# Optimization experiments

Measured on AMD Instinct MI355X. Metric: run time of the kernel, lower is better.

Reference implementation:

```python
import jax, jax.numpy as jnp
import numpy as np

B, T, CIN, HID, OUT, H, W = 8, 8, 128, 64, 64, 32, 32


def _conv(x, w, b):
    # x: [B, C, H, W], w: [O, C, kh, kw] -> SAME-padded conv, stride 1
    y = jax.lax.conv_general_dilated(x, w, (1, 1), "SAME",
                                     dimension_numbers=("NCHW", "OIHW", "NCHW"))
    return y + b[None, :, None, None]


def _layer_dir(xs, w_ih, w_hh, b_ih, b_hh, reverse):
    # xs: [T, B, C, H, W]; one direction of a ConvLSTM layer; returns hs [T, B, HID, H, W]
    b, hh_, ww_ = xs.shape[1], xs.shape[3], xs.shape[4]
    h0 = jnp.zeros((b, HID, hh_, ww_), xs.dtype)

    def step(carry, x):
        h, c = carry
        gates = _conv(x, w_ih, b_ih) + _conv(h, w_hh, b_hh)  # [B, 4*HID, H, W]
        i, f, g, o = jnp.split(gates, 4, axis=1)
        c = jax.nn.sigmoid(f) * c + jax.nn.sigmoid(i) * jnp.tanh(g)
        h = jax.nn.sigmoid(o) * jnp.tanh(c)
        return (h, c), h

    _, hs = jax.lax.scan(step, (h0, h0), xs, reverse=reverse)
    return hs


def _forward(features, w_ih0f, w_hh0f, b_ih0f, b_hh0f,
             w_ih0r, w_hh0r, b_ih0r, b_hh0r,
             w_ih1f, w_hh1f, b_ih1f, b_hh1f,
             w_ih1r, w_hh1r, b_ih1r, b_hh1r,
             w_out, b_out):
    xs = jnp.transpose(features, (1, 0, 2, 3, 4))  # [T, B, C, H, W]
    # layer 0, both directions (scan reverse=True aligns outputs to original time order)
    hf = _layer_dir(xs, w_ih0f, w_hh0f, b_ih0f, b_hh0f, False)
    hr = _layer_dir(xs, w_ih0r, w_hh0r, b_ih0r, b_hh0r, True)
    xs1 = jnp.concatenate([hf, hr], axis=2)  # [T, B, 2*HID, H, W] (dropout is identity at eval)
    # layer 1
    hf1 = _layer_dir(xs1, w_ih1f, w_hh1f, b_ih1f, b_hh1f, False)
    hr1 = _layer_dir(xs1, w_ih1r, w_hh1r, b_ih1r, b_hh1r, True)
    last = jnp.concatenate([hf1[-1], hr1[-1]], axis=1)  # output[:, -1] -> [B, 2*HID, H, W]
    return jax.nn.relu(_conv(last, w_out, b_out))


def setup_inputs() -> dict:
    key = jax.random.key(0)
    ks = jax.random.split(key, 24)
    G = 4 * HID
    p = lambda k, s: jax.random.normal(k, s, jnp.float32) * 0.05
    d = {"features": jax.random.normal(ks[0], (B, T, CIN, H, W), jnp.float32)}
    i = 1
    for l, cin in ((0, CIN), (1, 2 * HID)):
        for dr in ("f", "r"):
            d[f"w_ih{l}{dr}"] = p(ks[i], (G, cin, 3, 3)); i += 1
            d[f"w_hh{l}{dr}"] = p(ks[i], (G, HID, 3, 3)); i += 1
            d[f"b_ih{l}{dr}"] = p(ks[i], (G,)); i += 1
            d[f"b_hh{l}{dr}"] = p(ks[i], (G,)); i += 1
    d["w_out"] = p(ks[i], (OUT, 2 * HID, 1, 1)); i += 1
    d["b_out"] = p(ks[i], (OUT,))
    return d


def reference(features, w_ih0f, w_hh0f, b_ih0f, b_hh0f,
              w_ih0r, w_hh0r, b_ih0r, b_hh0r,
              w_ih1f, w_hh1f, b_ih1f, b_hh1f,
              w_ih1r, w_hh1r, b_ih1r, b_hh1r,
              w_out, b_out):
    return _forward(features, w_ih0f, w_hh0f, b_ih0f, b_hh0f,
                    w_ih0r, w_hh0r, b_ih0r, b_hh0r,
                    w_ih1f, w_hh1f, b_ih1f, b_hh1f,
                    w_ih1r, w_hh1r, b_ih1r, b_hh1r,
                    w_out, b_out)
```

## Files before the change

### kernel.cpp

```cpp
#include <hip/hip_runtime.h>
#include <math.h>
#include <stdint.h>


typedef __attribute__((ext_vector_type(8))) short short8;
typedef __attribute__((ext_vector_type(4))) float float4v;

namespace {
constexpr int IMG = 34 * 34 * 64;
constexpr size_t SLOTI = 16ull * IMG;
constexpr int ROWB = 34 * 128;
constexpr int PADB = 8192;
constexpr size_t GSLOT = 8ull * 256 * 1024;
constexpr int CGU32 = 73728;
}
template <int N> struct IC { static constexpr int v = N; };

__device__ __forceinline__ uint16_t bf16_rne(float x) {
  uint32_t u = __builtin_bit_cast(uint32_t, x);
  return (uint16_t)((u + 0x7FFFu + ((u >> 16) & 1u)) >> 16);
}
__device__ __forceinline__ float bf16_to_f(uint16_t h) {
  uint32_t u = ((uint32_t)h) << 16;
  return __builtin_bit_cast(float, u);
}

__device__ __forceinline__ void gl_lds16(const void* g, void* l) {
  __builtin_amdgcn_global_load_lds(
      (const __attribute__((address_space(1))) void*)g,
      (__attribute__((address_space(3))) void*)l, 16, 0, 0);
}

__global__ void pack_features(const float* __restrict__ f, uint16_t* __restrict__ out) {
  const size_t i = (size_t)blockIdx.x * 256 + threadIdx.x;
  const int blk_s = (int)(i & 7);
  size_t pp = i >> 3;
  const int px = (int)(pp % 34); pp /= 34;
  const int yy = (int)(pp % 34); pp /= 34;
  const int cg = (int)(pp & 3);
  const int bt = (int)(pp >> 2);
  const int b = bt & 7, t = bt >> 3;
  const int blk = blk_s ^ (px & 7);
  const int pl = blk >> 2, kg = blk & 3;
  short8 sv;
  if (px == 0 || px == 33 || yy == 0 || yy == 33) {
    #pragma unroll
    for (int j = 0; j < 8; ++j) sv[j] = 0;
  } else {
    const int x = px - 1, y = yy - 1;
    #pragma unroll
    for (int j = 0; j < 8; ++j) {
      const int ch = cg * 32 + kg * 8 + j;
      const float fv = f[(((size_t)b * 8 + t) * 128 + ch) * 1024 + y * 32 + x];
      const uint16_t hi = bf16_rne(fv);
      sv[j] = (short)(pl ? bf16_rne(fv - bf16_to_f(hi)) : hi);
    }
  }
  *(short8*)(out + i * 8) = sv;
}

struct WPackArgs {
  const float* wih[4]; const float* whh[4];
  const float* bih[4]; const float* bhh[4];
  uint32_t* wp; float* bp;
};
__global__ void pack_weights(WPackArgs A) {
  const int combo = blockIdx.y;
  const int idx = blockIdx.x * 256 + threadIdx.x;
  const int q = idx & 4095;
  const int rest = idx >> 12;
  const int nt = rest & 1;
  const int ct = rest >> 1;
  const int tap = ct % 9, cg = ct / 9;
  const int w2 = q & 3;
  const int b8s = (q >> 2) & 7;
  const int hcp = (q >> 5) & 15;
  const int g = (q >> 9) & 3;
  const int pl = (q >> 11) & 1;
  const int b8 = b8s ^ (hcp & 7);
  const int kg = b8 & 3;
  const int hcl = hcp * 2 + (b8 >> 2);
  const int n = g * 64 + nt * 32 + hcl;
  const float* wih = A.wih[combo];
  const float* whh = A.whh[combo];
  uint32_t out = 0;
  #pragma unroll
  for (int e = 0; e < 2; ++e) {
    const int ch = cg * 32 + kg * 8 + w2 * 2 + e;
    const float wv = (ch < 128) ? wih[((size_t)n * 128 + ch) * 9 + tap]
                                : whh[((size_t)n * 64 + (ch - 128)) * 9 + tap];
    const uint16_t hi = bf16_rne(wv);
    const uint16_t v = pl ? bf16_rne(wv - bf16_to_f(hi)) : hi;
    out |= ((uint32_t)v) << (16 * e);
  }
  A.wp[(size_t)combo * 442368 + idx] = out;
  if (idx < 256) A.bp[combo * 256 + idx] = A.bih[combo][idx] + A.bhh[combo][idx];
}

struct StepArgs {
  const uint16_t* in0; const uint16_t* in1; const uint16_t* in2;
  int nc0, nc1, nc2;
  const uint32_t* W;
  const float* bias;
  const float* gpre;
  float* cbuf;
  uint16_t* himg;
  float* hf32;
};

template <int ROWS>
__global__ __launch_bounds__(ROWS * 128, ROWS / 2) void conv_lstm_step(StepArgs A0, StepArgs A1) {
  constexpr int NW = ROWS * 2;
  constexpr int THREADS = NW * 64;
  constexpr int BANDS = 32 / ROWS;
  constexpr int LOGB = (ROWS == 4) ? 3 : 4;
  constexpr int ACH = (ROWS == 4) ? 4 : 5;
  constexpr int ASLOT = ACH * NW * 1024;
  constexpr int WCH = 16384 / (NW * 1024);
  constexpr int CNT0 = WCH;
  constexpr int CNT12 = WCH + ACH;

  extern __shared__ char smem[];
  char* Asm_ = smem;
  char* Wsm_ = smem + 2 * ASLOT;

  const StepArgs a = (blockIdx.z == 0) ? A0 : A1;
  const int bx = blockIdx.x;
  const int nt = bx & 1;
  const int band = (bx >> 1) & (BANDS - 1);
  const int b = bx >> (1 + LOGB);
  const int y0 = band * ROWS;
  const int tid = threadIdx.x;
  const int lane = tid & 63;
  const int w = tid >> 6;
  const int m15 = lane & 15;
  const int kg = lane >> 4;
  const int r = w & (ROWS - 1);
  const int hcg = (ROWS == 4) ? (w >> 2) : (w >> 1);

  int offA[2][3][2];
  #pragma unroll
  for (int xh = 0; xh < 2; ++xh)
    #pragma unroll
    for (int kx = 0; kx < 3; ++kx)
      #pragma unroll
      for (int pl = 0; pl < 2; ++pl) {
        const int px = xh * 16 + kx + m15;
        const int sw = (pl * 4 + kg) ^ (px & 7);
        offA[xh][kx][pl] = r * ROWB + px * 128 + sw * 16;
      }
  int offW[2][4];
  {
    const int hcp = hcg * 8 + (m15 >> 1);
    const int b8 = kg + 4 * (m15 & 1);
    #pragma unroll
    for (int pl = 0; pl < 2; ++pl)
      #pragma unroll
      for (int g = 0; g < 4; ++g)
        offW[pl][g] = (((pl * 4 + g) * 16 + hcp) * 8 + (b8 ^ (hcp & 7))) * 16;
  }

  const int ncg = a.nc0 + a.nc1 + a.nc2;
  auto abase = [&](int cg) -> const char* {
    const uint16_t* t;
    if (cg < a.nc0) t = a.in0 + ((size_t)b * a.nc0 + cg) * IMG;
    else if (cg < a.nc0 + a.nc1) t = a.in1 + ((size_t)b * a.nc1 + (cg - a.nc0)) * IMG;
    else t = a.in2 + ((size_t)b * a.nc2 + (cg - a.nc0 - a.nc1)) * IMG;
    return (const char*)t + (size_t)y0 * ROWB;
  };
  auto stageA = [&](int cgi, int par) {
    const char* g = abase(cgi);
    char* d = Asm_ + par * ASLOT;
    #pragma unroll
    for (int j = 0; j < ACH; ++j)
      gl_lds16(g + (size_t)(ACH * w + j) * 1024 + lane * 16, d + (ACH * w + j) * 1024);
  };
  const char* const wbeg = (const char*)a.W + (size_t)nt * 16384;
  const char* const wend = (const char*)a.W + (size_t)(ncg > 0 ? ncg : 1) * 9 * 32768;
  const char* wsrc = wbeg;
  auto stageW = [&](int slot) {
    char* d = Wsm_ + slot * 16384;
    #pragma unroll
    for (int j = 0; j < WCH; ++j)
      gl_lds16(wsrc + (size_t)(WCH * w + j) * 1024 + lane * 16, d + (WCH * w + j) * 1024);
    wsrc += 32768;
    if (wsrc >= wend) wsrc = wbeg;
  };

  float4v acc[2][4];
  #pragma unroll
  for (int xh = 0; xh < 2; ++xh)
    #pragma unroll
    for (int g = 0; g < 4; ++g) acc[xh][g] = (float4v){0.f, 0.f, 0.f, 0.f};

  if (ncg > 0) {
    stageA(0, 0);
    stageW(0);
    stageW(1);

    for (int cg = 0; cg < ncg; ++cg) {
      auto tap_body = [&](auto tapc) {
        constexpr int TAP = decltype(tapc)::v;
        constexpr int CNT = (TAP == 1 || TAP == 2) ? CNT12 : CNT0;
        constexpr int SLOT2 = (TAP + 2) % 3;
        constexpr int SLOTR = TAP % 3;
        asm volatile("s_waitcnt vmcnt(%0)\n\ts_barrier" :: "n"(CNT) : "memory");
        stageW(SLOT2);
        if (TAP == 0) {
          const int nx = (cg + 1 < ncg) ? cg + 1 : 0;
          stageA(nx, (cg + 1) & 1);
        }
        constexpr int ky = TAP / 3, kx = TAP % 3;
        const char* Ab = Asm_ + (cg & 1) * ASLOT + ky * ROWB;
        const char* Wb = Wsm_ + SLOTR * 16384;
        short8 af[2][2];
        #pragma unroll
        for (int xh = 0; xh < 2; ++xh)
          #pragma unroll
          for (int pl = 0; pl < 2; ++pl)
            af[xh][pl] = *(const short8*)(Ab + offA[xh][kx][pl]);
        short8 wfr[2][4];
        #pragma unroll
        for (int pl = 0; pl < 2; ++pl)
          #pragma unroll
          for (int g = 0; g < 4; ++g)
            wfr[pl][g] = *(const short8*)(Wb + offW[pl][g]);
        __builtin_amdgcn_s_setprio(1);
        #pragma unroll
        for (int xh = 0; xh < 2; ++xh)
          #pragma unroll
          for (int g = 0; g < 4; ++g) {
            acc[xh][g] = __builtin_amdgcn_mfma_f32_16x16x32_bf16(af[xh][0], wfr[0][g], acc[xh][g], 0, 0, 0);
            acc[xh][g] = __builtin_amdgcn_mfma_f32_16x16x32_bf16(af[xh][0], wfr[1][g], acc[xh][g], 0, 0, 0);
            acc[xh][g] = __builtin_amdgcn_mfma_f32_16x16x32_bf16(af[xh][1], wfr[0][g], acc[xh][g], 0, 0, 0);
          }
        __builtin_amdgcn_s_setprio(0);
      };
      tap_body(IC<0>{}); tap_body(IC<1>{}); tap_body(IC<2>{});
      tap_body(IC<3>{}); tap_body(IC<4>{}); tap_body(IC<5>{});
      tap_body(IC<6>{}); tap_body(IC<7>{}); tap_body(IC<8>{});
    }
    asm volatile("s_waitcnt vmcnt(0)" ::: "memory");
  }

  const int hcl = hcg * 16 + m15;
  const int hc = nt * 32 + hcl;
  const int y = y0 + r;
  float bi[4];
  #pragma unroll
  for (int g = 0; g < 4; ++g) bi[g] = a.bias[g * 64 + hc];
  float* crow = a.cbuf + ((size_t)(b * 64 + hc)) * 1024 + y * 32;
  float* hrow = a.hf32 ? a.hf32 + ((size_t)(b * 64 + hc)) * 1024 + y * 32 : nullptr;
  uint16_t* hb = a.himg ? a.himg + ((size_t)(b * 2 + nt)) * IMG : nullptr;
  const int kgb = hcl >> 3, jj = hcl & 7;
  #pragma unroll
  for (int xh = 0; xh < 2; ++xh) {
    const int x0 = xh * 16 + kg * 4;
    float4v cv = *(float4v*)(crow + x0);
    float4v pre[4];
    if (a.gpre) {
      #pragma unroll
      for (int g = 0; g < 4; ++g)
        pre[g] = *(const float4v*)(a.gpre + ((size_t)(b * 256 + g * 64 + hc)) * 1024 + y * 32 + x0);
    } else {
      #pragma unroll
      for (int g = 0; g < 4; ++g) pre[g] = (float4v){bi[g], bi[g], bi[g], bi[g]};
    }
    float4v cn, hn;
    #pragma unroll
    for (int q = 0; q < 4; ++q) {
      const float ig = 1.f / (1.f + expf(-(acc[xh][0][q] + pre[0][q])));
      const float fg = 1.f / (1.f + expf(-(acc[xh][1][q] + pre[1][q])));
      const float gg = tanhf(acc[xh][2][q] + pre[2][q]);
      const float og = 1.f / (1.f + expf(-(acc[xh][3][q] + pre[3][q])));
      const float c2 = fg * cv[q] + ig * gg;
      cn[q] = c2;
      hn[q] = og * tanhf(c2);
    }
    *(float4v*)(crow + x0) = cn;
    if (hrow) *(float4v*)(hrow + x0) = hn;
    if (hb) {
      #pragma unroll
      for (int q = 0; q < 4; ++q) {
        const int px = x0 + q + 1;
        const int sw = px & 7;
        const uint16_t hi = bf16_rne(hn[q]);
        const uint16_t lo = bf16_rne(hn[q] - bf16_to_f(hi));
        const size_t p16 = ((size_t)(y + 1) * 34 + px) * 64;
        hb[p16 + (size_t)(kgb ^ sw) * 8 + jj] = hi;
        hb[p16 + (size_t)((4 + kgb) ^ sw) * 8 + jj] = lo;
      }
    }
  }
  if (hb) {
    {
      const int rr = tid >> 7;
      const int hlf = (tid >> 6) & 1;
      const int jx = tid & 63;
      hb[((size_t)(y0 + 1 + rr) * 34 + hlf * 33) * 64 + jx] = 0;
    }
    if (band == 0) for (int i = tid; i < 2176; i += THREADS) hb[i] = 0;
    if (band == BANDS - 1) for (int i = tid; i < 2176; i += THREADS) hb[(size_t)33 * 2176 + i] = 0;
  }
}

struct PreArgs {
  const uint16_t* hf0i; const uint16_t* hr0i;
  const uint32_t* WP; const float* bp; float* gpre;
};
__global__ __launch_bounds__(512, 2) void conv_gates_pre(PreArgs P) {
  constexpr int ACH = 4, ASLOT = 32768, WCH = 2, CNT0 = 2, CNT12 = 6;
  extern __shared__ char smem[];
  char* Asm_ = smem;
  char* Wsm_ = smem + 65536;

  const int slot = blockIdx.y;
  const uint16_t* in0; const uint16_t* in1; const uint32_t* Wc; const float* bias;
  if (slot < 8) {
    in0 = P.hf0i + (size_t)(slot + 1) * SLOTI; in1 = P.hr0i + (size_t)slot * SLOTI;
    Wc = P.WP + (size_t)2 * 442368; bias = P.bp + 2 * 256;
  } else {
    in0 = P.hf0i + (size_t)8 * SLOTI; in1 = P.hr0i + (size_t)7 * SLOTI;
    Wc = P.WP + (size_t)3 * 442368; bias = P.bp + 3 * 256;
  }

  const int bx = blockIdx.x;
  const int nt = bx & 1;
  const int band = (bx >> 1) & 7;
  const int b = bx >> 4;
  const int y0 = band * 4;
  const int tid = threadIdx.x;
  const int lane = tid & 63;
  const int w = tid >> 6;
  const int m15 = lane & 15;
  const int kg = lane >> 4;
  const int r = w & 3;
  const int hcg = w >> 2;

  int offA[2][3][2];
  #pragma unroll
  for (int xh = 0; xh < 2; ++xh)
    #pragma unroll
    for (int kx = 0; kx < 3; ++kx)
      #pragma unroll
      for (int pl = 0; pl < 2; ++pl) {
        const int px = xh * 16 + kx + m15;
        const int sw = (pl * 4 + kg) ^ (px & 7);
        offA[xh][kx][pl] = r * ROWB + px * 128 + sw * 16;
      }
  int offW[2][4];
  {
    const int hcp = hcg * 8 + (m15 >> 1);
    const int b8 = kg + 4 * (m15 & 1);
    #pragma unroll
    for (int pl = 0; pl < 2; ++pl)
      #pragma unroll
      for (int g = 0; g < 4; ++g)
        offW[pl][g] = (((pl * 4 + g) * 16 + hcp) * 8 + (b8 ^ (hcp & 7))) * 16;
  }

  auto abase = [&](int cg) -> const char* {
    const uint16_t* t = (cg < 2) ? in0 + ((size_t)b * 2 + cg) * IMG
                                 : in1 + ((size_t)b * 2 + (cg - 2)) * IMG;
    return (const char*)t + (size_t)y0 * ROWB;
  };
  auto stageA = [&](int cgi, int par) {
    const char* g = abase(cgi);
    char* d = Asm_ + par * ASLOT;
    #pragma unroll
    for (int j = 0; j < ACH; ++j)
      gl_lds16(g + (size_t)(ACH * w + j) * 1024 + lane * 16, d + (ACH * w + j) * 1024);
  };
  const char* const wbeg = (const char*)Wc + (size_t)nt * 16384;
  const char* const wend = (const char*)Wc + (size_t)4 * 9 * 32768;
  const char* wsrc = wbeg;
  auto stageW = [&](int slotw) {
    char* d = Wsm_ + slotw * 16384;
    #pragma unroll
    for (int j = 0; j < WCH; ++j)
      gl_lds16(wsrc + (size_t)(WCH * w + j) * 1024 + lane * 16, d + (WCH * w + j) * 1024);
    wsrc += 32768;
    if (wsrc >= wend) wsrc = wbeg;
  };

  float4v acc[2][4];
  #pragma unroll
  for (int xh = 0; xh < 2; ++xh)
    #pragma unroll
    for (int g = 0; g < 4; ++g) acc[xh][g] = (float4v){0.f, 0.f, 0.f, 0.f};

  stageA(0, 0);
  stageW(0);
  stageW(1);

  for (int cg = 0; cg < 4; ++cg) {
    auto tap_body = [&](auto tapc) {
      constexpr int TAP = decltype(tapc)::v;
      constexpr int CNT = (TAP == 1 || TAP == 2) ? CNT12 : CNT0;
      constexpr int SLOT2 = (TAP + 2) % 3;
      constexpr int SLOTR = TAP % 3;
      asm volatile("s_waitcnt vmcnt(%0)\n\ts_barrier" :: "n"(CNT) : "memory");
      stageW(SLOT2);
      if (TAP == 0) {
        const int nx = (cg + 1 < 4) ? cg + 1 : 0;
        stageA(nx, (cg + 1) & 1);
      }
      constexpr int ky = TAP / 3, kx = TAP % 3;
      const char* Ab = Asm_ + (cg & 1) * ASLOT + ky * ROWB;
      const char* Wb = Wsm_ + SLOTR * 16384;
      short8 af[2][2];
      #pragma unroll
      for (int xh = 0; xh < 2; ++xh)
        #pragma unroll
        for (int pl = 0; pl < 2; ++pl)
          af[xh][pl] = *(const short8*)(Ab + offA[xh][kx][pl]);
      short8 wfr[2][4];
      #pragma unroll
      for (int pl = 0; pl < 2; ++pl)
        #pragma unroll
        for (int g = 0; g < 4; ++g)
          wfr[pl][g] = *(const short8*)(Wb + offW[pl][g]);
      __builtin_amdgcn_s_setprio(1);
      #pragma unroll
      for (int xh = 0; xh < 2; ++xh)
        #pragma unroll
        for (int g = 0; g < 4; ++g) {
          acc[xh][g] = __builtin_amdgcn_mfma_f32_16x16x32_bf16(af[xh][0], wfr[0][g], acc[xh][g], 0, 0, 0);
          acc[xh][g] = __builtin_amdgcn_mfma_f32_16x16x32_bf16(af[xh][0], wfr[1][g], acc[xh][g], 0, 0, 0);
          acc[xh][g] = __builtin_amdgcn_mfma_f32_16x16x32_bf16(af[xh][1], wfr[0][g], acc[xh][g], 0, 0, 0);
        }
      __builtin_amdgcn_s_setprio(0);
    };
    tap_body(IC<0>{}); tap_body(IC<1>{}); tap_body(IC<2>{});
    tap_body(IC<3>{}); tap_body(IC<4>{}); tap_body(IC<5>{});
    tap_body(IC<6>{}); tap_body(IC<7>{}); tap_body(IC<8>{});
  }
  asm volatile("s_waitcnt vmcnt(0)" ::: "memory");

  const int hcl = hcg * 16 + m15;
  const int hc = nt * 32 + hcl;
  const int y = y0 + r;
  float* gb = P.gpre + (size_t)slot * GSLOT + (size_t)b * 262144;
  #pragma unroll
  for (int xh = 0; xh < 2; ++xh) {
    const int x0 = xh * 16 + kg * 4;
    #pragma unroll
    for (int g = 0; g < 4; ++g) {
      float4v v = acc[xh][g];
      const float bv = bias[g * 64 + hc];
      #pragma unroll
      for (int q = 0; q < 4; ++q) v[q] += bv;
      *(float4v*)(gb + ((size_t)(g * 64 + hc)) * 1024 + y * 32 + x0) = v;
    }
  }
}

__global__ void final_conv(const float* __restrict__ h1f_last, const float* __restrict__ h1r_last,
                           const float* __restrict__ wout, const float* __restrict__ bout,
                           float* __restrict__ out) {
  __shared__ float Ws[16 * 128];
  const int oq = blockIdx.y;
  for (int i = threadIdx.x; i < 16 * 128; i += 256) Ws[i] = wout[oq * 16 * 128 + i];
  __syncthreads();
  const int gp = blockIdx.x * 256 + threadIdx.x;
  const int b = gp >> 10, p = gp & 1023;
  float acc[16];
  #pragma unroll
  for (int o = 0; o < 16; ++o) acc[o] = bout[oq * 16 + o];
  for (int c = 0; c < 128; ++c) {
    const float xv = (c < 64) ? h1f_last[((size_t)b * 64 + c) * 1024 + p]
                              : h1r_last[((size_t)b * 64 + (c - 64)) * 1024 + p];
    #pragma unroll
    for (int o = 0; o < 16; ++o) acc[o] = fmaf(xv, Ws[o * 128 + c], acc[o]);
  }
  #pragma unroll
  for (int o = 0; o < 16; ++o) {
    const float v = acc[o];
    out[((size_t)b * 64 + oq * 16 + o) * 1024 + p] = v > 0.f ? v : 0.f;
  }
}

extern "C" void kernel_launch(void* const* d_in, const int* in_sizes, int n_in,
                              void* d_out, int out_size, void* d_ws, size_t ws_size,
                              hipStream_t stream) {
  char* p = (char*)d_ws;
  uint16_t* featImg = (uint16_t*)p; p += (size_t)8 * 8 * 4 * IMG * 2 + PADB;
  uint32_t* WP = (uint32_t*)p;      p += (size_t)4 * 442368 * 4;
  float* bp = (float*)p;            p += 4096;
  uint16_t* hf0i = (uint16_t*)p;    p += (size_t)9 * SLOTI * 2 + PADB;
  uint16_t* hr0i = (uint16_t*)p;    p += (size_t)9 * SLOTI * 2 + PADB;
  uint16_t* h1fi = (uint16_t*)p;    p += (size_t)2 * SLOTI * 2 + PADB;
  float* c0f = (float*)p;           p += (size_t)4 * 2097152;
  float* c0r = c0f + 524288;
  float* c1f = c0r + 524288;
  float* c1r = c1f + 524288;
  float* h1f8 = (float*)p;          p += 2097152;
  float* h1r8 = (float*)p;          p += 2097152;
  float* gpre = (float*)p;          p += (size_t)9 * GSLOT * 4;

  hipMemsetAsync(c0f, 0, (size_t)4 * 2097152, stream);

  pack_features<<<dim3(9248), 256, 0, stream>>>((const float*)d_in[0], featImg);

  WPackArgs wa;
  for (int combo = 0; combo < 4; ++combo) {
    const int base = 1 + combo * 4;
    wa.wih[combo] = (const float*)d_in[base];
    wa.whh[combo] = (const float*)d_in[base + 1];
    wa.bih[combo] = (const float*)d_in[base + 2];
    wa.bhh[combo] = (const float*)d_in[base + 3];
  }
  wa.wp = WP; wa.bp = bp;
  pack_weights<<<dim3(1728, 4), 256, 0, stream>>>(wa);

  constexpr int DYN4 = 2 * 32768 + 3 * 16384;
  constexpr int DYN2 = 2 * 20480 + 3 * 16384;
  (void)hipFuncSetAttribute((const void*)(conv_lstm_step<4>),
                            hipFuncAttributeMaxDynamicSharedMemorySize, DYN4);
  (void)hipFuncSetAttribute((const void*)(conv_lstm_step<2>),
                            hipFuncAttributeMaxDynamicSharedMemorySize, DYN2);
  (void)hipFuncSetAttribute((const void*)conv_gates_pre,
                            hipFuncAttributeMaxDynamicSharedMemorySize, DYN4);

  auto mk = [&](const uint16_t* i0, int n0, const uint16_t* i1, int n1,
                const uint16_t* i2, int n2, int combo, int cgskip, float* cb,
                uint16_t* himg, float* hf32, const float* gp) {
    StepArgs s;
    s.in0 = i0; s.in1 = i1; s.in2 = i2;
    s.nc0 = n0; s.nc1 = n1; s.nc2 = n2;
    s.W = WP + (size_t)combo * 442368 + (size_t)cgskip * CGU32;
    s.bias = bp + combo * 256;
    s.gpre = gp; s.cbuf = cb; s.himg = himg; s.hf32 = hf32;
    return s;
  };

  for (int k = 0; k < 8; ++k) {
    const int tr = 7 - k;
    StepArgs f = (k == 0)
        ? mk(featImg, 4, nullptr, 0, nullptr, 0,
             0, 0, c0f, hf0i + (size_t)1 * SLOTI, nullptr, nullptr)
        : mk(featImg + (size_t)k * 8 * 4 * IMG, 4,
             hf0i + (size_t)k * SLOTI, 2, nullptr, 0,
             0, 0, c0f, hf0i + (size_t)(k + 1) * SLOTI, nullptr, nullptr);
    StepArgs r = (k == 0)
        ? mk(featImg + (size_t)7 * 8 * 4 * IMG, 4, nullptr, 0, nullptr, 0,
             1, 0, c0r, hr0i + (size_t)7 * SLOTI, nullptr, nullptr)
        : mk(featImg + (size_t)tr * 8 * 4 * IMG, 4,
             hr0i + (size_t)(tr + 1) * SLOTI, 2, nullptr, 0,
             1, 0, c0r, hr0i + (size_t)tr * SLOTI, nullptr, nullptr);
    conv_lstm_step<4><<<dim3(128, 1, 2), 512, DYN4, stream>>>(f, r);
  }

  PreArgs pa; pa.hf0i = hf0i; pa.hr0i = hr0i; pa.WP = WP; pa.bp = bp; pa.gpre = gpre;
  conv_gates_pre<<<dim3(128, 9), 512, DYN4, stream>>>(pa);

  {
    StepArgs f0 = mk(nullptr, 0, nullptr, 0, nullptr, 0,
                     2, 0, c1f, h1fi + (size_t)1 * SLOTI, nullptr, gpre);
    StepArgs rv = mk(nullptr, 0, nullptr, 0, nullptr, 0,
                     3, 0, c1r, nullptr, h1r8, gpre + (size_t)8 * GSLOT);
    conv_lstm_step<4><<<dim3(128, 1, 2), 512, DYN4, stream>>>(f0, rv);
  }

  for (int t = 1; t < 8; ++t) {
    uint16_t* himg = (t < 7) ? h1fi + (size_t)((t + 1) & 1) * SLOTI : nullptr;
    float* hf32 = (t == 7) ? h1f8 : nullptr;
    StepArgs s = mk(h1fi + (size_t)(t & 1) * SLOTI, 2, nullptr, 0, nullptr, 0,
                    2, 4, c1f, himg, hf32, gpre + (size_t)t * GSLOT);
    conv_lstm_step<2><<<dim3(256, 1, 1), 256, DYN2, stream>>>(s, s);
  }

  final_conv<<<dim3(32, 4), 256, 0, stream>>>(
      h1f8, h1r8, (const float*)d_in[17], (const float*)d_in[18], (float*)d_out);
}
```

Baseline: 717.4 us.

## Read conv weight fragments directly from global memory instead of staging through LDS

Result: slower. 783.2 us (+9.2%).

```diff
diff --git a/kernel.cpp b/kernel.cpp
--- a/kernel.cpp
+++ b/kernel.cpp
@@ -116,13 +116,9 @@
   constexpr int LOGB = (ROWS == 4) ? 3 : 4;
   constexpr int ACH = (ROWS == 4) ? 4 : 5;
   constexpr int ASLOT = ACH * NW * 1024;
-  constexpr int WCH = 16384 / (NW * 1024);
-  constexpr int CNT0 = WCH;
-  constexpr int CNT12 = WCH + ACH;
 
   extern __shared__ char smem[];
   char* Asm_ = smem;
-  char* Wsm_ = smem + 2 * ASLOT;
 
   const StepArgs a = (blockIdx.z == 0) ? A0 : A1;
   const int bx = blockIdx.x;
@@ -175,17 +171,6 @@
     for (int j = 0; j < ACH; ++j)
       gl_lds16(g + (size_t)(ACH * w + j) * 1024 + lane * 16, d + (ACH * w + j) * 1024);
   };
-  const char* const wbeg = (const char*)a.W + (size_t)nt * 16384;
-  const char* const wend = (const char*)a.W + (size_t)(ncg > 0 ? ncg : 1) * 9 * 32768;
-  const char* wsrc = wbeg;
-  auto stageW = [&](int slot) {
-    char* d = Wsm_ + slot * 16384;
-    #pragma unroll
-    for (int j = 0; j < WCH; ++j)
-      gl_lds16(wsrc + (size_t)(WCH * w + j) * 1024 + lane * 16, d + (WCH * w + j) * 1024);
-    wsrc += 32768;
-    if (wsrc >= wend) wsrc = wbeg;
-  };
 
   float4v acc[2][4];
   #pragma unroll
@@ -194,25 +179,21 @@
     for (int g = 0; g < 4; ++g) acc[xh][g] = (float4v){0.f, 0.f, 0.f, 0.f};
 
   if (ncg > 0) {
+    const char* wsrc = (const char*)a.W + (size_t)nt * 16384;
     stageA(0, 0);
-    stageW(0);
-    stageW(1);
 
     for (int cg = 0; cg < ncg; ++cg) {
+      asm volatile("s_waitcnt vmcnt(0)" ::: "memory");
+      __builtin_amdgcn_s_barrier();
+      {
+        const int nx = (cg + 1 < ncg) ? cg + 1 : 0;
+        stageA(nx, (cg + 1) & 1);
+      }
+      const char* Apar = Asm_ + (cg & 1) * ASLOT;
       auto tap_body = [&](auto tapc) {
         constexpr int TAP = decltype(tapc)::v;
-        constexpr int CNT = (TAP == 1 || TAP == 2) ? CNT12 : CNT0;
-        constexpr int SLOT2 = (TAP + 2) % 3;
-        constexpr int SLOTR = TAP % 3;
-        asm volatile("s_waitcnt vmcnt(%0)\n\ts_barrier" :: "n"(CNT) : "memory");
-        stageW(SLOT2);
-        if (TAP == 0) {
-          const int nx = (cg + 1 < ncg) ? cg + 1 : 0;
-          stageA(nx, (cg + 1) & 1);
-        }
         constexpr int ky = TAP / 3, kx = TAP % 3;
-        const char* Ab = Asm_ + (cg & 1) * ASLOT + ky * ROWB;
-        const char* Wb = Wsm_ + SLOTR * 16384;
+        const char* Ab = Apar + ky * ROWB;
         short8 af[2][2];
         #pragma unroll
         for (int xh = 0; xh < 2; ++xh)
@@ -224,7 +205,7 @@
         for (int pl = 0; pl < 2; ++pl)
           #pragma unroll
           for (int g = 0; g < 4; ++g)
-            wfr[pl][g] = *(const short8*)(Wb + offW[pl][g]);
+            wfr[pl][g] = *(const short8*)(wsrc + offW[pl][g]);
         __builtin_amdgcn_s_setprio(1);
         #pragma unroll
         for (int xh = 0; xh < 2; ++xh)
@@ -235,6 +216,7 @@
             acc[xh][g] = __builtin_amdgcn_mfma_f32_16x16x32_bf16(af[xh][1], wfr[0][g], acc[xh][g], 0, 0, 0);
           }
         __builtin_amdgcn_s_setprio(0);
+        wsrc += 32768;
       };
       tap_body(IC<0>{}); tap_body(IC<1>{}); tap_body(IC<2>{});
       tap_body(IC<3>{}); tap_body(IC<4>{}); tap_body(IC<5>{});
@@ -309,10 +291,9 @@
   const uint32_t* WP; const float* bp; float* gpre;
 };
 __global__ __launch_bounds__(512, 2) void conv_gates_pre(PreArgs P) {
-  constexpr int ACH = 4, ASLOT = 32768, WCH = 2, CNT0 = 2, CNT12 = 6;
+  constexpr int ACH = 4, ASLOT = 32768;
   extern __shared__ char smem[];
   char* Asm_ = smem;
-  char* Wsm_ = smem + 65536;
 
   const int slot = blockIdx.y;
   const uint16_t* in0; const uint16_t* in1; const uint32_t* Wc; const float* bias;
@@ -371,17 +352,6 @@
     for (int j = 0; j < ACH; ++j)
       gl_lds16(g + (size_t)(ACH * w + j) * 1024 + lane * 16, d + (ACH * w + j) * 1024);
   };
-  const char* const wbeg = (const char*)Wc + (size_t)nt * 16384;
-  const char* const wend = (const char*)Wc + (size_t)4 * 9 * 32768;
-  const char* wsrc = wbeg;
-  auto stageW = [&](int slotw) {
-    char* d = Wsm_ + slotw * 16384;
-    #pragma unroll
-    for (int j = 0; j < WCH; ++j)
-      gl_lds16(wsrc + (size_t)(WCH * w + j) * 1024 + lane * 16, d + (WCH * w + j) * 1024);
-    wsrc += 32768;
-    if (wsrc >= wend) wsrc = wbeg;
-  };
 
   float4v acc[2][4];
   #pragma unroll
@@ -389,25 +359,21 @@
     #pragma unroll
     for (int g = 0; g < 4; ++g) acc[xh][g] = (float4v){0.f, 0.f, 0.f, 0.f};
 
+  const char* wsrc = (const char*)Wc + (size_t)nt * 16384;
   stageA(0, 0);
-  stageW(0);
-  stageW(1);
 
   for (int cg = 0; cg < 4; ++cg) {
+    asm volatile("s_waitcnt vmcnt(0)" ::: "memory");
+    __builtin_amdgcn_s_barrier();
+    {
+      const int nx = (cg + 1 < 4) ? cg + 1 : 0;
+      stageA(nx, (cg + 1) & 1);
+    }
+    const char* Apar = Asm_ + (cg & 1) * ASLOT;
     auto tap_body = [&](auto tapc) {
       constexpr int TAP = decltype(tapc)::v;
-      constexpr int CNT = (TAP == 1 || TAP == 2) ? CNT12 : CNT0;
-      constexpr int SLOT2 = (TAP + 2) % 3;
-      constexpr int SLOTR = TAP % 3;
-      asm volatile("s_waitcnt vmcnt(%0)\n\ts_barrier" :: "n"(CNT) : "memory");
-      stageW(SLOT2);
-      if (TAP == 0) {
-        const int nx = (cg + 1 < 4) ? cg + 1 : 0;
-        stageA(nx, (cg + 1) & 1);
-      }
       constexpr int ky = TAP / 3, kx = TAP % 3;
-      const char* Ab = Asm_ + (cg & 1) * ASLOT + ky * ROWB;
-      const char* Wb = Wsm_ + SLOTR * 16384;
+      const char* Ab = Apar + ky * ROWB;
       short8 af[2][2];
       #pragma unroll
       for (int xh = 0; xh < 2; ++xh)
@@ -419,7 +385,7 @@
       for (int pl = 0; pl < 2; ++pl)
         #pragma unroll
         for (int g = 0; g < 4; ++g)
-          wfr[pl][g] = *(const short8*)(Wb + offW[pl][g]);
+          wfr[pl][g] = *(const short8*)(wsrc + offW[pl][g]);
       __builtin_amdgcn_s_setprio(1);
       #pragma unroll
       for (int xh = 0; xh < 2; ++xh)
@@ -430,6 +396,7 @@
           acc[xh][g] = __builtin_amdgcn_mfma_f32_16x16x32_bf16(af[xh][1], wfr[0][g], acc[xh][g], 0, 0, 0);
         }
       __builtin_amdgcn_s_setprio(0);
+      wsrc += 32768;
     };
     tap_body(IC<0>{}); tap_body(IC<1>{}); tap_body(IC<2>{});
     tap_body(IC<3>{}); tap_body(IC<4>{}); tap_body(IC<5>{});
@@ -513,8 +480,8 @@
   wa.wp = WP; wa.bp = bp;
   pack_weights<<<dim3(1728, 4), 256, 0, stream>>>(wa);
 
-  constexpr int DYN4 = 2 * 32768 + 3 * 16384;
-  constexpr int DYN2 = 2 * 20480 + 3 * 16384;
+  constexpr int DYN4 = 2 * 32768;
+  constexpr int DYN2 = 2 * 20480;
   (void)hipFuncSetAttribute((const void*)(conv_lstm_step<4>),
                             hipFuncAttributeMaxDynamicSharedMemorySize, DYN4);
   (void)hipFuncSetAttribute((const void*)(conv_lstm_step<2>),
```

## Add dedicated hidden-only ConvLSTM step kernel for layer-1 forward recurrence

Applied to the files above, without the earlier changes.

Measured after the change: 727.6 us. Within noise of the previous version (+1.4%).

```diff
diff --git a/kernel.cpp b/kernel.cpp
--- a/kernel.cpp
+++ b/kernel.cpp
@@ -304,6 +304,165 @@
   }
 }
 
+__global__ __launch_bounds__(512, 2) void conv_lstm_solo(StepArgs a) {
+  constexpr int ACH = 4, ASLOT = 32768;
+  extern __shared__ char smem[];
+  char* Asm_ = smem;
+  char* Wsm_ = smem + 2 * ASLOT;
+
+  const int bx = blockIdx.x;
+  const int Q4 = bx & 3;
+  const int band = (bx >> 2) & 7;
+  const int b = bx >> 5;
+  const int nt = Q4 >> 1, nq = Q4 & 1;
+  const int y0 = band * 4;
+  const int tid = threadIdx.x;
+  const int lane = tid & 63;
+  const int w = tid >> 6;
+  const int m15 = lane & 15;
+  const int kg = lane >> 4;
+  const int r = w & 3;
+  const int xh = w >> 2;
+
+  int offA[3][2];
+  #pragma unroll
+  for (int kx = 0; kx < 3; ++kx)
+    #pragma unroll
+    for (int pl = 0; pl < 2; ++pl) {
+      const int px = xh * 16 + kx + m15;
+      const int sw = (pl * 4 + kg) ^ (px & 7);
+      offA[kx][pl] = r * ROWB + px * 128 + sw * 16;
+    }
+  int offW[2][4];
+  {
+    const int hcpl = m15 >> 1;
+    const int b8 = kg + 4 * (m15 & 1);
+    #pragma unroll
+    for (int pl = 0; pl < 2; ++pl)
+      #pragma unroll
+      for (int g = 0; g < 4; ++g)
+        offW[pl][g] = (((pl * 4 + g) * 8 + hcpl) * 8 + (b8 ^ hcpl)) * 16;
+  }
+
+  auto abase = [&](int cg) -> const char* {
+    return (const char*)(a.in0 + ((size_t)b * 2 + cg) * IMG) + (size_t)y0 * ROWB;
+  };
+  auto stageA = [&](int cgi, int par) {
+    const char* g = abase(cgi);
+    char* d = Asm_ + par * ASLOT;
+    #pragma unroll
+    for (int j = 0; j < ACH; ++j)
+      gl_lds16(g + (size_t)(ACH * w + j) * 1024 + lane * 16, d + (ACH * w + j) * 1024);
+  };
+  const char* const wbeg = (const char*)a.W + (size_t)nt * 16384 + (size_t)nq * 1024;
+  const char* const wend = (const char*)a.W + (size_t)2 * 9 * 32768;
+  const char* wsrc = wbeg;
+  auto stageW = [&](int slot) {
+    gl_lds16(wsrc + (size_t)w * 2048 + lane * 16, Wsm_ + slot * 8192 + w * 1024);
+    wsrc += 32768;
+    if (wsrc >= wend) wsrc = wbeg;
+  };
+
+  float4v acc[4];
+  #pragma unroll
+  for (int g = 0; g < 4; ++g) acc[g] = (float4v){0.f, 0.f, 0.f, 0.f};
+
+  stageA(0, 0);
+  stageW(0);
+  stageW(1);
+
+  for (int cg = 0; cg < 2; ++cg) {
+    auto tap_body = [&](auto tapc) {
+      constexpr int TAP = decltype(tapc)::v;
+      constexpr int CNT = (TAP == 1 || TAP == 2) ? 5 : 1;
+      constexpr int SLOT2 = (TAP + 2) % 3;
+      constexpr int SLOTR = TAP % 3;
+      asm volatile("s_waitcnt vmcnt(%0)\n\ts_barrier" :: "n"(CNT) : "memory");
+      stageW(SLOT2);
+      if (TAP == 0) {
+        const int nx = (cg + 1 < 2) ? cg + 1 : 0;
+        stageA(nx, (cg + 1) & 1);
+      }
+      constexpr int ky = TAP / 3, kx = TAP % 3;
+      const char* Ab = Asm_ + (cg & 1) * ASLOT + ky * ROWB;
+      const char* Wb = Wsm_ + SLOTR * 8192;
+      short8 af[2];
+      #pragma unroll
+      for (int pl = 0; pl < 2; ++pl)
+        af[pl] = *(const short8*)(Ab + offA[kx][pl]);
+      short8 wfr[2][4];
+      #pragma unroll
+      for (int pl = 0; pl < 2; ++pl)
+        #pragma unroll
+        for (int g = 0; g < 4; ++g)
+          wfr[pl][g] = *(const short8*)(Wb + offW[pl][g]);
+      __builtin_amdgcn_s_setprio(1);
+      #pragma unroll
+      for (int g = 0; g < 4; ++g) {
+        acc[g] = __builtin_amdgcn_mfma_f32_16x16x32_bf16(af[0], wfr[0][g], acc[g], 0, 0, 0);
+        acc[g] = __builtin_amdgcn_mfma_f32_16x16x32_bf16(af[0], wfr[1][g], acc[g], 0, 0, 0);
+        acc[g] = __builtin_amdgcn_mfma_f32_16x16x32_bf16(af[1], wfr[0][g], acc[g], 0, 0, 0);
+      }
+      __builtin_amdgcn_s_setprio(0);
+    };
+    tap_body(IC<0>{}); tap_body(IC<1>{}); tap_body(IC<2>{});
+    tap_body(IC<3>{}); tap_body(IC<4>{}); tap_body(IC<5>{});
+    tap_body(IC<6>{}); tap_body(IC<7>{}); tap_body(IC<8>{});
+  }
+  asm volatile("s_waitcnt vmcnt(0)" ::: "memory");
+
+  const int hc = Q4 * 16 + m15;
+  const int y = y0 + r;
+  const int x0 = xh * 16 + kg * 4;
+  float* crow = a.cbuf + ((size_t)(b * 64 + hc)) * 1024 + y * 32;
+  float* hrow = a.hf32 ? a.hf32 + ((size_t)(b * 64 + hc)) * 1024 + y * 32 : nullptr;
+  uint16_t* hb = a.himg ? a.himg + ((size_t)(b * 2 + nt)) * IMG : nullptr;
+  const int chi = nq * 16 + m15;
+  const int kgb = chi >> 3, jj = chi & 7;
+  {
+    float4v cv = *(float4v*)(crow + x0);
+    float4v pre[4];
+    #pragma unroll
+    for (int g = 0; g < 4; ++g)
+      pre[g] = *(const float4v*)(a.gpre + ((size_t)(b * 256 + g * 64 + hc)) * 1024 + y * 32 + x0);
+    float4v cn, hn;
+    #pragma unroll
+    for (int q = 0; q < 4; ++q) {
+      const float ig = 1.f / (1.f + expf(-(acc[0][q] + pre[0][q])));
+      const float fg = 1.f / (1.f + expf(-(acc[1][q] + pre[1][q])));
+      const float gg = tanhf(acc[2][q] + pre[2][q]);
+      const float og = 1.f / (1.f + expf(-(acc[3][q] + pre[3][q])));
+      const float c2 = fg * cv[q] + ig * gg;
+      cn[q] = c2;
+      hn[q] = og * tanhf(c2);
+    }
+    *(float4v*)(crow + x0) = cn;
+    if (hrow) *(float4v*)(hrow + x0) = hn;
+    if (hb) {
+      #pragma unroll
+      for (int q = 0; q < 4; ++q) {
+        const int px = x0 + q + 1;
+        const int sw = px & 7;
+        const uint16_t hi = bf16_rne(hn[q]);
+        const uint16_t lo = bf16_rne(hn[q] - bf16_to_f(hi));
+        const size_t p16 = ((size_t)(y + 1) * 34 + px) * 64;
+        hb[p16 + (size_t)(kgb ^ sw) * 8 + jj] = hi;
+        hb[p16 + (size_t)((4 + kgb) ^ sw) * 8 + jj] = lo;
+      }
+    }
+  }
+  if (hb) {
+    {
+      const int rr = tid >> 7;
+      const int hlf = (tid >> 6) & 1;
+      const int jx = tid & 63;
+      hb[((size_t)(y0 + 1 + rr) * 34 + hlf * 33) * 64 + jx] = 0;
+    }
+    if (band == 0) for (int i = tid; i < 2176; i += 512) hb[i] = 0;
+    if (band == 7) for (int i = tid; i < 2176; i += 512) hb[(size_t)33 * 2176 + i] = 0;
+  }
+}
+
 struct PreArgs {
   const uint16_t* hf0i; const uint16_t* hr0i;
   const uint32_t* WP; const float* bp; float* gpre;
@@ -514,11 +673,11 @@
   pack_weights<<<dim3(1728, 4), 256, 0, stream>>>(wa);
 
   constexpr int DYN4 = 2 * 32768 + 3 * 16384;
-  constexpr int DYN2 = 2 * 20480 + 3 * 16384;
+  constexpr int DYNS = 2 * 32768 + 3 * 8192;
   (void)hipFuncSetAttribute((const void*)(conv_lstm_step<4>),
                             hipFuncAttributeMaxDynamicSharedMemorySize, DYN4);
-  (void)hipFuncSetAttribute((const void*)(conv_lstm_step<2>),
-                            hipFuncAttributeMaxDynamicSharedMemorySize, DYN2);
+  (void)hipFuncSetAttribute((const void*)conv_lstm_solo,
+                            hipFuncAttributeMaxDynamicSharedMemorySize, DYNS);
   (void)hipFuncSetAttribute((const void*)conv_gates_pre,
                             hipFuncAttributeMaxDynamicSharedMemorySize, DYN4);
 
@@ -567,7 +726,7 @@
     float* hf32 = (t == 7) ? h1f8 : nullptr;
     StepArgs s = mk(h1fi + (size_t)(t & 1) * SLOTI, 2, nullptr, 0, nullptr, 0,
                     2, 4, c1f, himg, hf32, gpre + (size_t)t * GSLOT);
-    conv_lstm_step<2><<<dim3(256, 1, 1), 256, DYN2, stream>>>(s, s);
+    conv_lstm_solo<<<dim3(256), 512, DYNS, stream>>>(s);
   }
 
   final_conv<<<dim3(32, 4), 256, 0, stream>>>(
```
